# Kernel optimization log

Measured on AMD Instinct MI355X. Metric: run time of the kernel, lower is better.

The kernel has to match this reference:

```python
import jax, jax.numpy as jnp
import numpy as np

RES, K, H = 8192, 48, 128

def _layer_norm(x, g, b, eps=1e-5):
    mu = jnp.mean(x, axis=-1, keepdims=True)
    var = jnp.var(x, axis=-1, keepdims=True)
    return (x - mu) * jax.lax.rsqrt(var + eps) * g + b

def _gelu(x):
    return jax.nn.gelu(x, approximate=False)  # torch default exact GELU

def setup_inputs() -> dict:
    key = jax.random.key(0)
    ks = jax.random.split(key, 16)
    s = 0.05
    inp = {
        "node_h": jax.random.normal(ks[0], (RES, H), jnp.float32),
        "edge_h": jax.random.normal(ks[1], (RES, K, H), jnp.float32),
        "edge_idx": jax.random.randint(ks[2], (RES, K), 0, RES, jnp.int32),
        "seq_emb": jax.random.normal(ks[3], (RES, H), jnp.float32),
        "ar_mask": jax.random.uniform(ks[4], (RES, K), jnp.float32),
        # msg_mlp: Linear(4h,h) -> GELU -> Linear(h,h) -> GELU -> Linear(h,h)
        "mW1": jax.random.normal(ks[5], (4 * H, H), jnp.float32) * s,
        "mb1": jnp.zeros((H,), jnp.float32),
        "mW2": jax.random.normal(ks[6], (H, H), jnp.float32) * s,
        "mb2": jnp.zeros((H,), jnp.float32),
        "mW3": jax.random.normal(ks[7], (H, H), jnp.float32) * s,
        "mb3": jnp.zeros((H,), jnp.float32),
        # ff_node: Linear(h,4h) -> GELU -> Linear(4h,h)
        "fW1": jax.random.normal(ks[8], (H, 4 * H), jnp.float32) * s,
        "fb1": jnp.zeros((4 * H,), jnp.float32),
        "fW2": jax.random.normal(ks[9], (4 * H, H), jnp.float32) * s,
        "fb2": jnp.zeros((H,), jnp.float32),
        "g1": jnp.ones((H,), jnp.float32), "b1": jnp.zeros((H,), jnp.float32),
        "g2": jnp.ones((H,), jnp.float32), "b2": jnp.zeros((H,), jnp.float32),
    }
    return inp

def reference(node_h, edge_h, edge_idx, seq_emb, ar_mask,
              mW1, mb1, mW2, mb2, mW3, mb3,
              fW1, fb1, fW2, fb2, g1, b1, g2, b2):
    seq_j = seq_emb[edge_idx] * ar_mask[..., None]           # [res,k,h]
    e_dec = jnp.concatenate([edge_h, seq_j], axis=-1)        # [res,k,2h]
    h_j = node_h[edge_idx]                                   # [res,k,h]
    h_i = jnp.broadcast_to(node_h[:, None, :], (node_h.shape[0], edge_idx.shape[1], node_h.shape[1]))
    x = jnp.concatenate([h_i, h_j, e_dec], axis=-1)          # [res,k,4h]
    msg = _gelu(x @ mW1 + mb1)
    msg = _gelu(msg @ mW2 + mb2)
    msg = msg @ mW3 + mb3                                    # [res,k,h]
    agg = jnp.sum(msg, axis=1)                               # [res,h]
    h = _layer_norm(node_h + agg, g1, b1)
    ff = _gelu(h @ fW1 + fb1) @ fW2 + fb2
    h = _layer_norm(h + ff, g2, b2)
    return h
```

## Files before the change

### kernel.cpp

```cpp
#include <hip/hip_runtime.h>

#define KNB 48

typedef float  floatx4 __attribute__((ext_vector_type(4)));
typedef __bf16 bf16x8  __attribute__((ext_vector_type(8)));
typedef unsigned short ushort8  __attribute__((ext_vector_type(8)));
typedef unsigned short ushort4v __attribute__((ext_vector_type(4)));

__device__ __forceinline__ float bf2f(unsigned short b) {
  union { unsigned int u; float f; } v; v.u = ((unsigned int)b) << 16; return v.f;
}
__device__ __forceinline__ unsigned short f2bf(float f) {
  __bf16 h = (__bf16)f;
  union { __bf16 h; unsigned short u; } v; v.h = h; return v.u;
}
__device__ __forceinline__ float gelu_f(float x) {
  float u = x * (0.7978845608f + 0.0356774081f * x * x);
  float t = __builtin_amdgcn_exp2f(u * -2.8853900818f);
  return x * __builtin_amdgcn_rcpf(1.0f + t);
}

__global__ __launch_bounds__(256) void k0_transpose(
    const float* mW1, const float* mW2, const float* mW3,
    const float* fW1, const float* fW2,
    unsigned short* MT1, unsigned short* WT2, unsigned short* WT3,
    unsigned short* FWT1, unsigned short* FWT2) {
  __shared__ unsigned short tile[32][33];
  int b = blockIdx.x;
  const float* src; unsigned short* dst; int Kd, Nd, t;
  if (b < 64)       { src = mW1; dst = MT1;  Kd = 512; Nd = 128; t = b; }
  else if (b < 80)  { src = mW2; dst = WT2;  Kd = 128; Nd = 128; t = b - 64; }
  else if (b < 96)  { src = mW3; dst = WT3;  Kd = 128; Nd = 128; t = b - 80; }
  else if (b < 160) { src = fW1; dst = FWT1; Kd = 128; Nd = 512; t = b - 96; }
  else              { src = fW2; dst = FWT2; Kd = 512; Nd = 128; t = b - 160; }
  int tN = Nd >> 5;
  int tk = t / tN, tn = t % tN;
  int tx = threadIdx.x & 31, ty = threadIdx.x >> 5;
  for (int r = 0; r < 4; ++r) {
    int row = ty + r * 8;
    tile[row][tx] = f2bf(src[(size_t)(tk * 32 + row) * Nd + tn * 32 + tx]);
  }
  __syncthreads();
  for (int r = 0; r < 4; ++r) {
    int row = ty + r * 8;
    dst[(size_t)(tn * 32 + row) * Kd + tk * 32 + tx] = tile[tx][row];
  }
}

__global__ __launch_bounds__(256) void k1_nodepre(
    const float* node_h, const float* seq_emb,
    const unsigned short* MT1, const float* mb1,
    float* Apr, unsigned short* BS) {
  __shared__ __align__(16) unsigned short sX[2][32 * 128];
  int r0 = blockIdx.x * 32;
  int tid = threadIdx.x, lane = tid & 63, w = tid >> 6;
  int l15 = lane & 15, l16 = lane >> 4;

  for (int mset = 0; mset < 2; ++mset) {
    const float* src = mset ? (seq_emb + (size_t)r0 * 128) : (node_h + (size_t)r0 * 128);
    for (int k = 0; k < 4; ++k) {
      int f = tid + 256 * k;
      floatx4 v = ((const floatx4*)src)[f];
      int row = f >> 5, hc = f & 31, c = hc >> 1, half = hc & 1;
      ushort4v o;
      o[0] = f2bf(v[0]); o[1] = f2bf(v[1]); o[2] = f2bf(v[2]); o[3] = f2bf(v[3]);
      *(ushort4v*)((char*)&sX[mset][0] + row * 256 + ((c ^ (row & 7)) << 4) + half * 8) = o;
    }
  }
  __syncthreads();

  for (int q = 0; q < 6; ++q) {
    int job = w + 4 * q;
    int kind = job >> 3;
    int nt = job & 7;
    int colOff = (kind == 0) ? 0 : (kind == 1) ? 128 : 384;
    const unsigned short* X = sX[kind == 2 ? 1 : 0];
    bf16x8 wf[4];
    for (int kk = 0; kk < 4; ++kk)
      wf[kk] = *(const bf16x8*)(MT1 + (size_t)(nt * 16 + l15) * 512 + colOff + kk * 32 + l16 * 8);
    for (int mt = 0; mt < 2; ++mt) {
      floatx4 acc = {0.f, 0.f, 0.f, 0.f};
      for (int kk = 0; kk < 4; ++kk) {
        int row = mt * 16 + l15;
        int off = (kk * 64 + l16 * 16) ^ ((row & 7) << 4);
        bf16x8 a = *(const bf16x8*)((const char*)X + row * 256 + off);
        acc = __builtin_amdgcn_mfma_f32_16x16x32_bf16(a, wf[kk], acc, 0, 0, 0);
      }
      int col = nt * 16 + l15;
      for (int r = 0; r < 4; ++r) {
        int row = r0 + mt * 16 + l16 * 4 + r;
        if (kind == 0)      Apr[(size_t)row * 128 + col] = acc[r] + mb1[col];
        else if (kind == 1) BS[(size_t)row * 256 + col] = f2bf(acc[r]);
        else                BS[(size_t)row * 256 + 128 + col] = f2bf(acc[r]);
      }
    }
  }
}

__global__ __launch_bounds__(512) void k2_edge(
    const float* edge_h, const int* edge_idx, const float* ar_mask,
    const unsigned short* MT1, const unsigned short* WT2, const unsigned short* WT3,
    const float* mb2, const float* mb3,
    const float* Apr, const unsigned short* BS,
    float* agg) {
  __shared__ __align__(16) unsigned short sE[96 * 128];
  __shared__ __align__(16) unsigned short sT[96 * 128];
  int i0 = blockIdx.x * 2;
  int tid = threadIdx.x, lane = tid & 63, w = tid >> 6;
  int l15 = lane & 15, l16 = lane >> 4;
  int rb = (l16 & 1) * 4;
  int colw = w * 16 + l15;
  int cp = ((colw >> 3) << 4) | ((l15 & 7) << 1);

  const float* eb = edge_h + (size_t)i0 * KNB * 128;
#pragma unroll
  for (int k = 0; k < 6; ++k) {
    int f = tid + 512 * k;
    floatx4 v = ((const floatx4*)eb)[f];
    int row = f >> 5, hc = f & 31, c = hc >> 1, half = hc & 1;
    ushort4v o;
    o[0] = f2bf(v[0]); o[1] = f2bf(v[1]); o[2] = f2bf(v[2]); o[3] = f2bf(v[3]);
    *(ushort4v*)((char*)sE + row * 256 + ((c ^ (row & 7)) << 4) + half * 8) = o;
  }
#pragma unroll
  for (int k = 0; k < 3; ++k) {
    int u = tid + 512 * k;
    int e = u >> 4, c8 = u & 15;
    int j = edge_idx[(size_t)i0 * KNB + e];
    float m = ar_mask[(size_t)i0 * KNB + e];
    int i = i0 + (e >= 48 ? 1 : 0);
    const floatx4* ap = (const floatx4*)(Apr + (size_t)i * 128 + c8 * 8);
    floatx4 a0 = ap[0], a1 = ap[1];
    ushort8 vb = *(const ushort8*)(BS + (size_t)j * 256 + c8 * 8);
    ushort8 vs = *(const ushort8*)(BS + (size_t)j * 256 + 128 + c8 * 8);
    ushort8 res;
#pragma unroll
    for (int x = 0; x < 4; ++x)
      res[x] = f2bf(a0[x] + bf2f(vb[x]) + m * bf2f(vs[x]));
#pragma unroll
    for (int x = 0; x < 4; ++x)
      res[4 + x] = f2bf(a1[x] + bf2f(vb[4 + x]) + m * bf2f(vs[4 + x]));
    *(ushort8*)((char*)sT + e * 256 + ((c8 ^ (e & 7)) * 16)) = res;
  }
  __syncthreads();

  {
    bf16x8 wf[4];
#pragma unroll
    for (int kk = 0; kk < 4; ++kk)
      wf[kk] = *(const bf16x8*)(MT1 + (size_t)colw * 512 + 256 + kk * 32 + l16 * 8);
    for (int mt = 0; mt < 6; ++mt) {
      floatx4 acc = {0.f,0.f,0.f,0.f};
#pragma unroll
      for (int kk = 0; kk < 4; ++kk) {
        int row = mt * 16 + l15;
        int off = (kk * 64 + l16 * 16) ^ ((row & 7) << 4);
        bf16x8 a = *(const bf16x8*)((const char*)sE + row * 256 + off);
        acc = __builtin_amdgcn_mfma_f32_16x16x32_bf16(a, wf[kk], acc, 0, 0, 0);
      }
      char* base = (char*)sT + (mt * 16 + l16 * 4) * 256;
#pragma unroll
      for (int r = 0; r < 4; ++r) {
        char* p = base + r * 256 + (cp ^ ((rb + r) << 4));
        float g = bf2f(*(unsigned short*)p);
        *(unsigned short*)p = f2bf(gelu_f(acc[r] + g));
      }
    }
  }
  __syncthreads();

  {
    bf16x8 wf[4];
#pragma unroll
    for (int kk = 0; kk < 4; ++kk)
      wf[kk] = *(const bf16x8*)(WT2 + (size_t)colw * 128 + kk * 32 + l16 * 8);
    float bb = mb2[colw];
    for (int mt = 0; mt < 6; ++mt) {
      floatx4 acc = {0.f,0.f,0.f,0.f};
#pragma unroll
      for (int kk = 0; kk < 4; ++kk) {
        int row = mt * 16 + l15;
        int off = (kk * 64 + l16 * 16) ^ ((row & 7) << 4);
        bf16x8 a = *(const bf16x8*)((const char*)sT + row * 256 + off);
        acc = __builtin_amdgcn_mfma_f32_16x16x32_bf16(a, wf[kk], acc, 0, 0, 0);
      }
      char* base = (char*)sE + (mt * 16 + l16 * 4) * 256;
#pragma unroll
      for (int r = 0; r < 4; ++r) {
        char* p = base + r * 256 + (cp ^ ((rb + r) << 4));
        *(unsigned short*)p = f2bf(gelu_f(acc[r] + bb));
      }
    }
  }
  __syncthreads();

  {
    bf16x8 wf[4];
#pragma unroll
    for (int kk = 0; kk < 4; ++kk)
      wf[kk] = *(const bf16x8*)(WT3 + (size_t)colw * 128 + kk * 32 + l16 * 8);
#pragma unroll
    for (int half = 0; half < 2; ++half) {
      float agga[4] = {0.f,0.f,0.f,0.f};
      for (int mt3 = 0; mt3 < 3; ++mt3) {
        int mt = half * 3 + mt3;
        floatx4 acc = {0.f,0.f,0.f,0.f};
#pragma unroll
        for (int kk = 0; kk < 4; ++kk) {
          int row = mt * 16 + l15;
          int off = (kk * 64 + l16 * 16) ^ ((row & 7) << 4);
          bf16x8 a = *(const bf16x8*)((const char*)sE + row * 256 + off);
          acc = __builtin_amdgcn_mfma_f32_16x16x32_bf16(a, wf[kk], acc, 0, 0, 0);
        }
#pragma unroll
        for (int r = 0; r < 4; ++r) agga[r] += acc[r];
      }
      float s = agga[0] + agga[1] + agga[2] + agga[3];
      s += __shfl_xor(s, 16);
      s += __shfl_xor(s, 32);
      if (lane < 16) {
        int col = w * 16 + lane;
        agg[(size_t)(i0 + half) * 128 + col] = s + 48.0f * mb3[col];
      }
    }
  }
}

__global__ __launch_bounds__(256) void k3_ff(
    const float* node_h, const float* agg,
    const unsigned short* FWT1, const unsigned short* FWT2,
    const float* fb1, const float* fb2,
    const float* g1, const float* b1,
    const float* g2, const float* b2,
    float* out) {
  __shared__ __align__(16) unsigned short sH[32 * 128];
  __shared__ __align__(16) unsigned short sT3[32 * 512];
  __shared__ float sP[32 * 128];
  int r0 = blockIdx.x * 32;
  int tid = threadIdx.x, lane = tid & 63, w = tid >> 6;
  int l15 = lane & 15, l16 = lane >> 4;

  {
    int row = tid >> 3;
    int c0 = (tid & 7) * 16;
    const floatx4* nh4 = (const floatx4*)(node_h + (size_t)(r0 + row) * 128 + c0);
    const floatx4* ag4 = (const floatx4*)(agg + (size_t)(r0 + row) * 128 + c0);
    float x[16]; float sum = 0.f, sum2 = 0.f;
#pragma unroll
    for (int q4 = 0; q4 < 4; ++q4) {
      floatx4 a = nh4[q4], g = ag4[q4];
#pragma unroll
      for (int j = 0; j < 4; ++j) {
        float xv = a[j] + g[j];
        x[q4 * 4 + j] = xv; sum += xv; sum2 += xv * xv;
      }
    }
    sum  += __shfl_xor(sum, 1);  sum  += __shfl_xor(sum, 2);  sum  += __shfl_xor(sum, 4);
    sum2 += __shfl_xor(sum2, 1); sum2 += __shfl_xor(sum2, 2); sum2 += __shfl_xor(sum2, 4);
    float mu = sum * (1.f / 128.f);
    float var = sum2 * (1.f / 128.f) - mu * mu;
    float rstd = rsqrtf(var + 1e-5f);
#pragma unroll
    for (int q = 0; q < 16; ++q) {
      int col = c0 + q;
      float h = (x[q] - mu) * rstd * g1[col] + b1[col];
      sP[row * 128 + col] = h;
      char* p = (char*)sH + row * 256 + ((((col >> 3) ^ (row & 7)) << 4) | ((col & 7) << 1));
      *(unsigned short*)p = f2bf(h);
    }
  }
  __syncthreads();

  for (int nq = 0; nq < 8; ++nq) {
    int nt = w * 8 + nq;
    bf16x8 wf[4];
    for (int kk = 0; kk < 4; ++kk)
      wf[kk] = *(const bf16x8*)(FWT1 + (size_t)(nt * 16 + l15) * 128 + kk * 32 + l16 * 8);
    for (int mt = 0; mt < 2; ++mt) {
      floatx4 acc = {0.f,0.f,0.f,0.f};
      for (int kk = 0; kk < 4; ++kk) {
        int row = mt * 16 + l15;
        int off = (kk * 64 + l16 * 16) ^ ((row & 7) << 4);
        bf16x8 a = *(const bf16x8*)((const char*)sH + row * 256 + off);
        acc = __builtin_amdgcn_mfma_f32_16x16x32_bf16(a, wf[kk], acc, 0, 0, 0);
      }
      int col = nt * 16 + l15;
      float bb = fb1[col];
      for (int r = 0; r < 4; ++r) {
        int row = mt * 16 + l16 * 4 + r;
        char* p = (char*)sT3 + row * 1024 + ((((col >> 3) ^ (row & 7)) << 4) | ((col & 7) << 1));
        *(unsigned short*)p = f2bf(gelu_f(acc[r] + bb));
      }
    }
  }
  __syncthreads();

  for (int n = 0; n < 2; ++n) {
    int nt = 2 * w + n;
    for (int mt = 0; mt < 2; ++mt) {
      floatx4 acc = {0.f,0.f,0.f,0.f};
      for (int kk = 0; kk < 16; ++kk) {
        int row = mt * 16 + l15;
        int off = (kk * 64 + l16 * 16) ^ ((row & 7) << 4);
        bf16x8 a = *(const bf16x8*)((const char*)sT3 + row * 1024 + off);
        bf16x8 b = *(const bf16x8*)(FWT2 + (size_t)(nt * 16 + l15) * 512 + kk * 32 + l16 * 8);
        acc = __builtin_amdgcn_mfma_f32_16x16x32_bf16(a, b, acc, 0, 0, 0);
      }
      int col = nt * 16 + l15;
      float bb = fb2[col];
      for (int r = 0; r < 4; ++r) {
        int row = mt * 16 + l16 * 4 + r;
        sP[row * 128 + col] += acc[r] + bb;
      }
    }
  }
  __syncthreads();

  {
    int row = tid >> 3;
    int c0 = (tid & 7) * 16;
    float x[16]; float sum = 0.f, sum2 = 0.f;
#pragma unroll
    for (int q = 0; q < 16; ++q) {
      float xv = sP[row * 128 + c0 + q];
      x[q] = xv; sum += xv; sum2 += xv * xv;
    }
    sum  += __shfl_xor(sum, 1);  sum  += __shfl_xor(sum, 2);  sum  += __shfl_xor(sum, 4);
    sum2 += __shfl_xor(sum2, 1); sum2 += __shfl_xor(sum2, 2); sum2 += __shfl_xor(sum2, 4);
    float mu = sum * (1.f / 128.f);
    float var = sum2 * (1.f / 128.f) - mu * mu;
    float rstd = rsqrtf(var + 1e-5f);
#pragma unroll
    for (int q = 0; q < 16; ++q) {
      int col = c0 + q;
      out[(size_t)(r0 + row) * 128 + col] = (x[q] - mu) * rstd * g2[col] + b2[col];
    }
  }
}

extern "C" void kernel_launch(void* const* d_in, const int* in_sizes, int n_in,
                              void* d_out, int out_size, void* d_ws, size_t ws_size,
                              hipStream_t stream) {
  const float* node_h  = (const float*)d_in[0];
  const float* edge_h  = (const float*)d_in[1];
  const int*   edge_idx= (const int*)d_in[2];
  const float* seq_emb = (const float*)d_in[3];
  const float* ar_mask = (const float*)d_in[4];
  const float* mW1 = (const float*)d_in[5];
  const float* mb1 = (const float*)d_in[6];
  const float* mW2 = (const float*)d_in[7];
  const float* mb2 = (const float*)d_in[8];
  const float* mW3 = (const float*)d_in[9];
  const float* mb3 = (const float*)d_in[10];
  const float* fW1 = (const float*)d_in[11];
  const float* fb1 = (const float*)d_in[12];
  const float* fW2 = (const float*)d_in[13];
  const float* fb2 = (const float*)d_in[14];
  const float* g1  = (const float*)d_in[15];
  const float* b1  = (const float*)d_in[16];
  const float* g2  = (const float*)d_in[17];
  const float* b2  = (const float*)d_in[18];

  char* ws = (char*)d_ws;
  unsigned short* MT1  = (unsigned short*)(ws + 0);
  unsigned short* WT2  = (unsigned short*)(ws + 131072);
  unsigned short* WT3  = (unsigned short*)(ws + 163840);
  unsigned short* FWT1 = (unsigned short*)(ws + 196608);
  unsigned short* FWT2 = (unsigned short*)(ws + 327680);
  float*          Apr  = (float*)(ws + 458752);
  unsigned short* BS   = (unsigned short*)(ws + 4653056);
  float*          agg  = (float*)(ws + 8847360);

  hipLaunchKernelGGL(k0_transpose, dim3(224), dim3(256), 0, stream,
                     mW1, mW2, mW3, fW1, fW2, MT1, WT2, WT3, FWT1, FWT2);
  hipLaunchKernelGGL(k1_nodepre, dim3(256), dim3(256), 0, stream,
                     node_h, seq_emb, MT1, mb1, Apr, BS);
  hipLaunchKernelGGL(k2_edge, dim3(4096), dim3(512), 0, stream,
                     edge_h, edge_idx, ar_mask, MT1, WT2, WT3, mb2, mb3,
                     Apr, BS, agg);
  hipLaunchKernelGGL(k3_ff, dim3(256), dim3(256), 0, stream,
                     node_h, agg, FWT1, FWT2, fb1, fb2, g1, b1, g2, b2,
                     (float*)d_out);
}
```

Baseline: 139.5 us.

## Retile edge MLP waves to 48 rows x 32 cols with split accumulators

In the edge kernel, each wave previously covered all 96 edge rows for one 16-column tile. It now covers one residue's 48 rows for two 16-column tiles, so each A fragment loaded from LDS feeds two MFMAs and LDS read traffic roughly halves. Each column tile also uses two independent accumulators, which breaks the MFMA dependency chain and exposes more instruction-level parallelism. The price is higher register use from two weight fragment sets, partly addressed by a launch_bounds occupancy hint of (512, 6). The final per-residue reduction no longer needs a loop over halves.

Result: slower. 191.8 us (+37.5%).

```diff
diff --git a/kernel.cpp b/kernel.cpp
--- a/kernel.cpp
+++ b/kernel.cpp
@@ -19,6 +19,8 @@
   float t = __builtin_amdgcn_exp2f(u * -2.8853900818f);
   return x * __builtin_amdgcn_rcpf(1.0f + t);
 }
+
+#define MFMA16(a, b, c) __builtin_amdgcn_mfma_f32_16x16x32_bf16((a), (b), (c), 0, 0, 0)
 
 __global__ __launch_bounds__(256) void k0_transpose(
     const float* mW1, const float* mW2, const float* mW3,
@@ -84,7 +86,7 @@
         int row = mt * 16 + l15;
         int off = (kk * 64 + l16 * 16) ^ ((row & 7) << 4);
         bf16x8 a = *(const bf16x8*)((const char*)X + row * 256 + off);
-        acc = __builtin_amdgcn_mfma_f32_16x16x32_bf16(a, wf[kk], acc, 0, 0, 0);
+        acc = MFMA16(a, wf[kk], acc);
       }
       int col = nt * 16 + l15;
       for (int r = 0; r < 4; ++r) {
@@ -97,7 +99,7 @@
   }
 }
 
-__global__ __launch_bounds__(512) void k2_edge(
+__global__ __launch_bounds__(512, 6) void k2_edge(
     const float* edge_h, const int* edge_idx, const float* ar_mask,
     const unsigned short* MT1, const unsigned short* WT2, const unsigned short* WT3,
     const float* mb2, const float* mb3,
@@ -108,9 +110,13 @@
   int i0 = blockIdx.x * 2;
   int tid = threadIdx.x, lane = tid & 63, w = tid >> 6;
   int l15 = lane & 15, l16 = lane >> 4;
+  int h = w >> 2;
+  int ntp = w & 3;
+  int R0 = h * 48;
+  int cA = ntp * 32 + l15, cB = cA + 16;
   int rb = (l16 & 1) * 4;
-  int colw = w * 16 + l15;
-  int cp = ((colw >> 3) << 4) | ((l15 & 7) << 1);
+  int cpA = ((cA >> 3) << 4) | ((l15 & 7) << 1);
+  int cpB = ((cB >> 3) << 4) | ((l15 & 7) << 1);
 
   const float* eb = edge_h + (size_t)i0 * KNB * 128;
 #pragma unroll
@@ -145,83 +151,113 @@
   __syncthreads();
 
   {
-    bf16x8 wf[4];
-#pragma unroll
-    for (int kk = 0; kk < 4; ++kk)
-      wf[kk] = *(const bf16x8*)(MT1 + (size_t)colw * 512 + 256 + kk * 32 + l16 * 8);
-    for (int mt = 0; mt < 6; ++mt) {
-      floatx4 acc = {0.f,0.f,0.f,0.f};
+    bf16x8 wfA[4], wfB[4];
+#pragma unroll
+    for (int kk = 0; kk < 4; ++kk) {
+      wfA[kk] = *(const bf16x8*)(MT1 + (size_t)cA * 512 + 256 + kk * 32 + l16 * 8);
+      wfB[kk] = *(const bf16x8*)(MT1 + (size_t)cB * 512 + 256 + kk * 32 + l16 * 8);
+    }
+#pragma unroll
+    for (int mt = 0; mt < 3; ++mt) {
+      bf16x8 af[4];
 #pragma unroll
       for (int kk = 0; kk < 4; ++kk) {
-        int row = mt * 16 + l15;
-        int off = (kk * 64 + l16 * 16) ^ ((row & 7) << 4);
-        bf16x8 a = *(const bf16x8*)((const char*)sE + row * 256 + off);
-        acc = __builtin_amdgcn_mfma_f32_16x16x32_bf16(a, wf[kk], acc, 0, 0, 0);
-      }
-      char* base = (char*)sT + (mt * 16 + l16 * 4) * 256;
-#pragma unroll
-      for (int r = 0; r < 4; ++r) {
-        char* p = base + r * 256 + (cp ^ ((rb + r) << 4));
-        float g = bf2f(*(unsigned short*)p);
-        *(unsigned short*)p = f2bf(gelu_f(acc[r] + g));
+        int row = R0 + mt * 16 + l15;
+        int off = (kk * 64 + l16 * 16) ^ ((row & 7) << 4);
+        af[kk] = *(const bf16x8*)((const char*)sE + row * 256 + off);
+      }
+      floatx4 aA0 = {0.f,0.f,0.f,0.f}, aA1 = {0.f,0.f,0.f,0.f};
+      floatx4 aB0 = {0.f,0.f,0.f,0.f}, aB1 = {0.f,0.f,0.f,0.f};
+      aA0 = MFMA16(af[0], wfA[0], aA0); aB0 = MFMA16(af[0], wfB[0], aB0);
+      aA1 = MFMA16(af[1], wfA[1], aA1); aB1 = MFMA16(af[1], wfB[1], aB1);
+      aA0 = MFMA16(af[2], wfA[2], aA0); aB0 = MFMA16(af[2], wfB[2], aB0);
+      aA1 = MFMA16(af[3], wfA[3], aA1); aB1 = MFMA16(af[3], wfB[3], aB1);
+      char* base = (char*)sT + (R0 + mt * 16 + l16 * 4) * 256;
+#pragma unroll
+      for (int r = 0; r < 4; ++r) {
+        int sw = (rb + r) << 4;
+        char* pA = base + r * 256 + (cpA ^ sw);
+        char* pB = base + r * 256 + (cpB ^ sw);
+        float gA = bf2f(*(unsigned short*)pA);
+        float gB = bf2f(*(unsigned short*)pB);
+        *(unsigned short*)pA = f2bf(gelu_f(aA0[r] + aA1[r] + gA));
+        *(unsigned short*)pB = f2bf(gelu_f(aB0[r] + aB1[r] + gB));
       }
     }
   }
   __syncthreads();
 
   {
-    bf16x8 wf[4];
-#pragma unroll
-    for (int kk = 0; kk < 4; ++kk)
-      wf[kk] = *(const bf16x8*)(WT2 + (size_t)colw * 128 + kk * 32 + l16 * 8);
-    float bb = mb2[colw];
-    for (int mt = 0; mt < 6; ++mt) {
-      floatx4 acc = {0.f,0.f,0.f,0.f};
+    bf16x8 wfA[4], wfB[4];
+#pragma unroll
+    for (int kk = 0; kk < 4; ++kk) {
+      wfA[kk] = *(const bf16x8*)(WT2 + (size_t)cA * 128 + kk * 32 + l16 * 8);
+      wfB[kk] = *(const bf16x8*)(WT2 + (size_t)cB * 128 + kk * 32 + l16 * 8);
+    }
+    float bbA = mb2[cA], bbB = mb2[cB];
+#pragma unroll
+    for (int mt = 0; mt < 3; ++mt) {
+      bf16x8 af[4];
 #pragma unroll
       for (int kk = 0; kk < 4; ++kk) {
-        int row = mt * 16 + l15;
-        int off = (kk * 64 + l16 * 16) ^ ((row & 7) << 4);
-        bf16x8 a = *(const bf16x8*)((const char*)sT + row * 256 + off);
-        acc = __builtin_amdgcn_mfma_f32_16x16x32_bf16(a, wf[kk], acc, 0, 0, 0);
-      }
-      char* base = (char*)sE + (mt * 16 + l16 * 4) * 256;
-#pragma unroll
-      for (int r = 0; r < 4; ++r) {
-        char* p = base + r * 256 + (cp ^ ((rb + r) << 4));
-        *(unsigned short*)p = f2bf(gelu_f(acc[r] + bb));
+        int row = R0 + mt * 16 + l15;
+        int off = (kk * 64 + l16 * 16) ^ ((row & 7) << 4);
+        af[kk] = *(const bf16x8*)((const char*)sT + row * 256 + off);
+      }
+      floatx4 aA0 = {0.f,0.f,0.f,0.f}, aA1 = {0.f,0.f,0.f,0.f};
+      floatx4 aB0 = {0.f,0.f,0.f,0.f}, aB1 = {0.f,0.f,0.f,0.f};
+      aA0 = MFMA16(af[0], wfA[0], aA0); aB0 = MFMA16(af[0], wfB[0], aB0);
+      aA1 = MFMA16(af[1], wfA[1], aA1); aB1 = MFMA16(af[1], wfB[1], aB1);
+      aA0 = MFMA16(af[2], wfA[2], aA0); aB0 = MFMA16(af[2], wfB[2], aB0);
+      aA1 = MFMA16(af[3], wfA[3], aA1); aB1 = MFMA16(af[3], wfB[3], aB1);
+      char* base = (char*)sE + (R0 + mt * 16 + l16 * 4) * 256;
+#pragma unroll
+      for (int r = 0; r < 4; ++r) {
+        int sw = (rb + r) << 4;
+        *(unsigned short*)(base + r * 256 + (cpA ^ sw)) = f2bf(gelu_f(aA0[r] + aA1[r] + bbA));
+        *(unsigned short*)(base + r * 256 + (cpB ^ sw)) = f2bf(gelu_f(aB0[r] + aB1[r] + bbB));
       }
     }
   }
   __syncthreads();
 
   {
-    bf16x8 wf[4];
-#pragma unroll
-    for (int kk = 0; kk < 4; ++kk)
-      wf[kk] = *(const bf16x8*)(WT3 + (size_t)colw * 128 + kk * 32 + l16 * 8);
-#pragma unroll
-    for (int half = 0; half < 2; ++half) {
-      float agga[4] = {0.f,0.f,0.f,0.f};
-      for (int mt3 = 0; mt3 < 3; ++mt3) {
-        int mt = half * 3 + mt3;
-        floatx4 acc = {0.f,0.f,0.f,0.f};
-#pragma unroll
-        for (int kk = 0; kk < 4; ++kk) {
-          int row = mt * 16 + l15;
-          int off = (kk * 64 + l16 * 16) ^ ((row & 7) << 4);
-          bf16x8 a = *(const bf16x8*)((const char*)sE + row * 256 + off);
-          acc = __builtin_amdgcn_mfma_f32_16x16x32_bf16(a, wf[kk], acc, 0, 0, 0);
-        }
-#pragma unroll
-        for (int r = 0; r < 4; ++r) agga[r] += acc[r];
-      }
-      float s = agga[0] + agga[1] + agga[2] + agga[3];
-      s += __shfl_xor(s, 16);
-      s += __shfl_xor(s, 32);
-      if (lane < 16) {
-        int col = w * 16 + lane;
-        agg[(size_t)(i0 + half) * 128 + col] = s + 48.0f * mb3[col];
-      }
+    bf16x8 wfA[4], wfB[4];
+#pragma unroll
+    for (int kk = 0; kk < 4; ++kk) {
+      wfA[kk] = *(const bf16x8*)(WT3 + (size_t)cA * 128 + kk * 32 + l16 * 8);
+      wfB[kk] = *(const bf16x8*)(WT3 + (size_t)cB * 128 + kk * 32 + l16 * 8);
+    }
+    float sumA[4] = {0.f,0.f,0.f,0.f}, sumB[4] = {0.f,0.f,0.f,0.f};
+#pragma unroll
+    for (int mt = 0; mt < 3; ++mt) {
+      bf16x8 af[4];
+#pragma unroll
+      for (int kk = 0; kk < 4; ++kk) {
+        int row = R0 + mt * 16 + l15;
+        int off = (kk * 64 + l16 * 16) ^ ((row & 7) << 4);
+        af[kk] = *(const bf16x8*)((const char*)sE + row * 256 + off);
+      }
+      floatx4 aA0 = {0.f,0.f,0.f,0.f}, aA1 = {0.f,0.f,0.f,0.f};
+      floatx4 aB0 = {0.f,0.f,0.f,0.f}, aB1 = {0.f,0.f,0.f,0.f};
+      aA0 = MFMA16(af[0], wfA[0], aA0); aB0 = MFMA16(af[0], wfB[0], aB0);
+      aA1 = MFMA16(af[1], wfA[1], aA1); aB1 = MFMA16(af[1], wfB[1], aB1);
+      aA0 = MFMA16(af[2], wfA[2], aA0); aB0 = MFMA16(af[2], wfB[2], aB0);
+      aA1 = MFMA16(af[3], wfA[3], aA1); aB1 = MFMA16(af[3], wfB[3], aB1);
+#pragma unroll
+      for (int r = 0; r < 4; ++r) {
+        sumA[r] += aA0[r] + aA1[r];
+        sumB[r] += aB0[r] + aB1[r];
+      }
+    }
+    float sA = sumA[0] + sumA[1] + sumA[2] + sumA[3];
+    float sB = sumB[0] + sumB[1] + sumB[2] + sumB[3];
+    sA += __shfl_xor(sA, 16); sA += __shfl_xor(sA, 32);
+    sB += __shfl_xor(sB, 16); sB += __shfl_xor(sB, 32);
+    if (lane < 16) {
+      int colA = ntp * 32 + lane, colB = colA + 16;
+      agg[(size_t)(i0 + h) * 128 + colA] = sA + 48.0f * mb3[colA];
+      agg[(size_t)(i0 + h) * 128 + colB] = sB + 48.0f * mb3[colB];
     }
   }
 }
@@ -282,7 +318,7 @@
         int row = mt * 16 + l15;
         int off = (kk * 64 + l16 * 16) ^ ((row & 7) << 4);
         bf16x8 a = *(const bf16x8*)((const char*)sH + row * 256 + off);
-        acc = __builtin_amdgcn_mfma_f32_16x16x32_bf16(a, wf[kk], acc, 0, 0, 0);
+        acc = MFMA16(a, wf[kk], acc);
       }
       int col = nt * 16 + l15;
       float bb = fb1[col];
@@ -304,7 +340,7 @@
         int off = (kk * 64 + l16 * 16) ^ ((row & 7) << 4);
         bf16x8 a = *(const bf16x8*)((const char*)sT3 + row * 1024 + off);
         bf16x8 b = *(const bf16x8*)(FWT2 + (size_t)(nt * 16 + l15) * 512 + kk * 32 + l16 * 8);
-        acc = __builtin_amdgcn_mfma_f32_16x16x32_bf16(a, b, acc, 0, 0, 0);
+        acc = MFMA16(a, b, acc);
       }
       int col = nt * 16 + l15;
       float bb = fb2[col];
```

## Make edge kernel persistent over four node pairs with register prefetch of next tile

Applied to the files above, without the earlier changes.

The edge kernel now processes four consecutive node pairs per block instead of one, which cuts the grid by a factor of four. For the next pair it prefetches edge_h, edge_idx and ar_mask into registers while the current pair's three MFMA layers run. The goal is to overlap the large edge_h stream with compute and amortise block launch and weight-fragment setup. The cost is more registers for the prefetch buffers, an extra barrier per iteration, and fewer blocks to spread across CUs; launch_bounds(512,4) is set to limit register use.

Result: slower. 147.2 us (+5.5%).

```diff
diff --git a/kernel.cpp b/kernel.cpp
--- a/kernel.cpp
+++ b/kernel.cpp
@@ -1,6 +1,7 @@
 #include <hip/hip_runtime.h>
 
 #define KNB 48
+#define NT  4
 
 typedef float  floatx4 __attribute__((ext_vector_type(4)));
 typedef __bf16 bf16x8  __attribute__((ext_vector_type(8)));
@@ -19,6 +20,8 @@
   float t = __builtin_amdgcn_exp2f(u * -2.8853900818f);
   return x * __builtin_amdgcn_rcpf(1.0f + t);
 }
+
+#define MFMA16(a, b, c) __builtin_amdgcn_mfma_f32_16x16x32_bf16((a), (b), (c), 0, 0, 0)
 
 __global__ __launch_bounds__(256) void k0_transpose(
     const float* mW1, const float* mW2, const float* mW3,
@@ -84,7 +87,7 @@
         int row = mt * 16 + l15;
         int off = (kk * 64 + l16 * 16) ^ ((row & 7) << 4);
         bf16x8 a = *(const bf16x8*)((const char*)X + row * 256 + off);
-        acc = __builtin_amdgcn_mfma_f32_16x16x32_bf16(a, wf[kk], acc, 0, 0, 0);
+        acc = MFMA16(a, wf[kk], acc);
       }
       int col = nt * 16 + l15;
       for (int r = 0; r < 4; ++r) {
@@ -97,7 +100,7 @@
   }
 }
 
-__global__ __launch_bounds__(512) void k2_edge(
+__global__ __launch_bounds__(512, 4) void k2_edge(
     const float* edge_h, const int* edge_idx, const float* ar_mask,
     const unsigned short* MT1, const unsigned short* WT2, const unsigned short* WT3,
     const float* mb2, const float* mb3,
@@ -105,124 +108,156 @@
     float* agg) {
   __shared__ __align__(16) unsigned short sE[96 * 128];
   __shared__ __align__(16) unsigned short sT[96 * 128];
-  int i0 = blockIdx.x * 2;
   int tid = threadIdx.x, lane = tid & 63, w = tid >> 6;
   int l15 = lane & 15, l16 = lane >> 4;
   int rb = (l16 & 1) * 4;
   int colw = w * 16 + l15;
   int cp = ((colw >> 3) << 4) | ((l15 & 7) << 1);
 
-  const float* eb = edge_h + (size_t)i0 * KNB * 128;
-#pragma unroll
-  for (int k = 0; k < 6; ++k) {
-    int f = tid + 512 * k;
-    floatx4 v = ((const floatx4*)eb)[f];
-    int row = f >> 5, hc = f & 31, c = hc >> 1, half = hc & 1;
-    ushort4v o;
-    o[0] = f2bf(v[0]); o[1] = f2bf(v[1]); o[2] = f2bf(v[2]); o[3] = f2bf(v[3]);
-    *(ushort4v*)((char*)sE + row * 256 + ((c ^ (row & 7)) << 4) + half * 8) = o;
-  }
-#pragma unroll
-  for (int k = 0; k < 3; ++k) {
-    int u = tid + 512 * k;
-    int e = u >> 4, c8 = u & 15;
-    int j = edge_idx[(size_t)i0 * KNB + e];
-    float m = ar_mask[(size_t)i0 * KNB + e];
-    int i = i0 + (e >= 48 ? 1 : 0);
-    const floatx4* ap = (const floatx4*)(Apr + (size_t)i * 128 + c8 * 8);
-    floatx4 a0 = ap[0], a1 = ap[1];
-    ushort8 vb = *(const ushort8*)(BS + (size_t)j * 256 + c8 * 8);
-    ushort8 vs = *(const ushort8*)(BS + (size_t)j * 256 + 128 + c8 * 8);
-    ushort8 res;
-#pragma unroll
-    for (int x = 0; x < 4; ++x)
-      res[x] = f2bf(a0[x] + bf2f(vb[x]) + m * bf2f(vs[x]));
-#pragma unroll
-    for (int x = 0; x < 4; ++x)
-      res[4 + x] = f2bf(a1[x] + bf2f(vb[4 + x]) + m * bf2f(vs[4 + x]));
-    *(ushort8*)((char*)sT + e * 256 + ((c8 ^ (e & 7)) * 16)) = res;
-  }
-  __syncthreads();
+  int p0 = blockIdx.x * NT;
+
+  floatx4 ev[6];
+  int   jr[3];
+  float mr[3];
 
   {
-    bf16x8 wf[4];
-#pragma unroll
-    for (int kk = 0; kk < 4; ++kk)
-      wf[kk] = *(const bf16x8*)(MT1 + (size_t)colw * 512 + 256 + kk * 32 + l16 * 8);
-    for (int mt = 0; mt < 6; ++mt) {
-      floatx4 acc = {0.f,0.f,0.f,0.f};
-#pragma unroll
-      for (int kk = 0; kk < 4; ++kk) {
-        int row = mt * 16 + l15;
-        int off = (kk * 64 + l16 * 16) ^ ((row & 7) << 4);
-        bf16x8 a = *(const bf16x8*)((const char*)sE + row * 256 + off);
-        acc = __builtin_amdgcn_mfma_f32_16x16x32_bf16(a, wf[kk], acc, 0, 0, 0);
-      }
-      char* base = (char*)sT + (mt * 16 + l16 * 4) * 256;
-#pragma unroll
-      for (int r = 0; r < 4; ++r) {
-        char* p = base + r * 256 + (cp ^ ((rb + r) << 4));
-        float g = bf2f(*(unsigned short*)p);
-        *(unsigned short*)p = f2bf(gelu_f(acc[r] + g));
-      }
-    }
-  }
-  __syncthreads();
-
-  {
-    bf16x8 wf[4];
-#pragma unroll
-    for (int kk = 0; kk < 4; ++kk)
-      wf[kk] = *(const bf16x8*)(WT2 + (size_t)colw * 128 + kk * 32 + l16 * 8);
-    float bb = mb2[colw];
-    for (int mt = 0; mt < 6; ++mt) {
-      floatx4 acc = {0.f,0.f,0.f,0.f};
-#pragma unroll
-      for (int kk = 0; kk < 4; ++kk) {
-        int row = mt * 16 + l15;
-        int off = (kk * 64 + l16 * 16) ^ ((row & 7) << 4);
-        bf16x8 a = *(const bf16x8*)((const char*)sT + row * 256 + off);
-        acc = __builtin_amdgcn_mfma_f32_16x16x32_bf16(a, wf[kk], acc, 0, 0, 0);
-      }
-      char* base = (char*)sE + (mt * 16 + l16 * 4) * 256;
-#pragma unroll
-      for (int r = 0; r < 4; ++r) {
-        char* p = base + r * 256 + (cp ^ ((rb + r) << 4));
-        *(unsigned short*)p = f2bf(gelu_f(acc[r] + bb));
-      }
-    }
-  }
-  __syncthreads();
-
-  {
-    bf16x8 wf[4];
-#pragma unroll
-    for (int kk = 0; kk < 4; ++kk)
-      wf[kk] = *(const bf16x8*)(WT3 + (size_t)colw * 128 + kk * 32 + l16 * 8);
-#pragma unroll
-    for (int half = 0; half < 2; ++half) {
-      float agga[4] = {0.f,0.f,0.f,0.f};
-      for (int mt3 = 0; mt3 < 3; ++mt3) {
-        int mt = half * 3 + mt3;
+    const float* eb = edge_h + (size_t)(p0 * 2) * KNB * 128;
+#pragma unroll
+    for (int k = 0; k < 6; ++k) ev[k] = ((const floatx4*)eb)[tid + 512 * k];
+#pragma unroll
+    for (int k = 0; k < 3; ++k) {
+      int e = (tid + 512 * k) >> 4;
+      jr[k] = edge_idx[(size_t)(p0 * 2) * KNB + e];
+      mr[k] = ar_mask[(size_t)(p0 * 2) * KNB + e];
+    }
+  }
+
+  for (int t = 0; t < NT; ++t) {
+    int i0 = (p0 + t) * 2;
+
+#pragma unroll
+    for (int k = 0; k < 6; ++k) {
+      int f = tid + 512 * k;
+      floatx4 v = ev[k];
+      int row = f >> 5, hc = f & 31, c = hc >> 1, half = hc & 1;
+      ushort4v o;
+      o[0] = f2bf(v[0]); o[1] = f2bf(v[1]); o[2] = f2bf(v[2]); o[3] = f2bf(v[3]);
+      *(ushort4v*)((char*)sE + row * 256 + ((c ^ (row & 7)) << 4) + half * 8) = o;
+    }
+#pragma unroll
+    for (int k = 0; k < 3; ++k) {
+      int u = tid + 512 * k;
+      int e = u >> 4, c8 = u & 15;
+      int j = jr[k]; float m = mr[k];
+      int i = i0 + (e >= 48 ? 1 : 0);
+      const floatx4* ap = (const floatx4*)(Apr + (size_t)i * 128 + c8 * 8);
+      floatx4 a0 = ap[0], a1 = ap[1];
+      ushort8 vb = *(const ushort8*)(BS + (size_t)j * 256 + c8 * 8);
+      ushort8 vs = *(const ushort8*)(BS + (size_t)j * 256 + 128 + c8 * 8);
+      ushort8 res;
+#pragma unroll
+      for (int x = 0; x < 4; ++x)
+        res[x] = f2bf(a0[x] + bf2f(vb[x]) + m * bf2f(vs[x]));
+#pragma unroll
+      for (int x = 0; x < 4; ++x)
+        res[4 + x] = f2bf(a1[x] + bf2f(vb[4 + x]) + m * bf2f(vs[4 + x]));
+      *(ushort8*)((char*)sT + e * 256 + ((c8 ^ (e & 7)) * 16)) = res;
+    }
+    __syncthreads();
+
+    if (t + 1 < NT) {
+      const float* eb = edge_h + (size_t)((p0 + t + 1) * 2) * KNB * 128;
+#pragma unroll
+      for (int k = 0; k < 6; ++k) ev[k] = ((const floatx4*)eb)[tid + 512 * k];
+#pragma unroll
+      for (int k = 0; k < 3; ++k) {
+        int e = (tid + 512 * k) >> 4;
+        jr[k] = edge_idx[(size_t)((p0 + t + 1) * 2) * KNB + e];
+        mr[k] = ar_mask[(size_t)((p0 + t + 1) * 2) * KNB + e];
+      }
+    }
+
+    {
+      bf16x8 wf[4];
+#pragma unroll
+      for (int kk = 0; kk < 4; ++kk)
+        wf[kk] = *(const bf16x8*)(MT1 + (size_t)colw * 512 + 256 + kk * 32 + l16 * 8);
+      for (int mt = 0; mt < 6; ++mt) {
         floatx4 acc = {0.f,0.f,0.f,0.f};
 #pragma unroll
         for (int kk = 0; kk < 4; ++kk) {
           int row = mt * 16 + l15;
           int off = (kk * 64 + l16 * 16) ^ ((row & 7) << 4);
           bf16x8 a = *(const bf16x8*)((const char*)sE + row * 256 + off);
-          acc = __builtin_amdgcn_mfma_f32_16x16x32_bf16(a, wf[kk], acc, 0, 0, 0);
-        }
-#pragma unroll
-        for (int r = 0; r < 4; ++r) agga[r] += acc[r];
-      }
-      float s = agga[0] + agga[1] + agga[2] + agga[3];
-      s += __shfl_xor(s, 16);
-      s += __shfl_xor(s, 32);
-      if (lane < 16) {
-        int col = w * 16 + lane;
-        agg[(size_t)(i0 + half) * 128 + col] = s + 48.0f * mb3[col];
-      }
-    }
+          acc = MFMA16(a, wf[kk], acc);
+        }
+        char* base = (char*)sT + (mt * 16 + l16 * 4) * 256;
+#pragma unroll
+        for (int r = 0; r < 4; ++r) {
+          char* p = base + r * 256 + (cp ^ ((rb + r) << 4));
+          float g = bf2f(*(unsigned short*)p);
+          *(unsigned short*)p = f2bf(gelu_f(acc[r] + g));
+        }
+      }
+    }
+    __syncthreads();
+
+    {
+      bf16x8 wf[4];
+#pragma unroll
+      for (int kk = 0; kk < 4; ++kk)
+        wf[kk] = *(const bf16x8*)(WT2 + (size_t)colw * 128 + kk * 32 + l16 * 8);
+      float bb = mb2[colw];
+      for (int mt = 0; mt < 6; ++mt) {
+        floatx4 acc = {0.f,0.f,0.f,0.f};
+#pragma unroll
+        for (int kk = 0; kk < 4; ++kk) {
+          int row = mt * 16 + l15;
+          int off = (kk * 64 + l16 * 16) ^ ((row & 7) << 4);
+          bf16x8 a = *(const bf16x8*)((const char*)sT + row * 256 + off);
+          acc = MFMA16(a, wf[kk], acc);
+        }
+        char* base = (char*)sE + (mt * 16 + l16 * 4) * 256;
+#pragma unroll
+        for (int r = 0; r < 4; ++r) {
+          char* p = base + r * 256 + (cp ^ ((rb + r) << 4));
+          *(unsigned short*)p = f2bf(gelu_f(acc[r] + bb));
+        }
+      }
+    }
+    __syncthreads();
+
+    {
+      bf16x8 wf[4];
+#pragma unroll
+      for (int kk = 0; kk < 4; ++kk)
+        wf[kk] = *(const bf16x8*)(WT3 + (size_t)colw * 128 + kk * 32 + l16 * 8);
+#pragma unroll
+      for (int half = 0; half < 2; ++half) {
+        float agga[4] = {0.f,0.f,0.f,0.f};
+        for (int mt3 = 0; mt3 < 3; ++mt3) {
+          int mt = half * 3 + mt3;
+          floatx4 acc = {0.f,0.f,0.f,0.f};
+#pragma unroll
+          for (int kk = 0; kk < 4; ++kk) {
+            int row = mt * 16 + l15;
+            int off = (kk * 64 + l16 * 16) ^ ((row & 7) << 4);
+            bf16x8 a = *(const bf16x8*)((const char*)sE + row * 256 + off);
+            acc = MFMA16(a, wf[kk], acc);
+          }
+#pragma unroll
+          for (int r = 0; r < 4; ++r) agga[r] += acc[r];
+        }
+        float s = agga[0] + agga[1] + agga[2] + agga[3];
+        s += __shfl_xor(s, 16);
+        s += __shfl_xor(s, 32);
+        if (lane < 16) {
+          int col = w * 16 + lane;
+          agg[(size_t)(i0 + half) * 128 + col] = s + 48.0f * mb3[col];
+        }
+      }
+    }
+    __syncthreads();
   }
 }
 
@@ -282,7 +317,7 @@
         int row = mt * 16 + l15;
         int off = (kk * 64 + l16 * 16) ^ ((row & 7) << 4);
         bf16x8 a = *(const bf16x8*)((const char*)sH + row * 256 + off);
-        acc = __builtin_amdgcn_mfma_f32_16x16x32_bf16(a, wf[kk], acc, 0, 0, 0);
+        acc = MFMA16(a, wf[kk], acc);
       }
       int col = nt * 16 + l15;
       float bb = fb1[col];
@@ -304,7 +339,7 @@
         int off = (kk * 64 + l16 * 16) ^ ((row & 7) << 4);
         bf16x8 a = *(const bf16x8*)((const char*)sT3 + row * 1024 + off);
         bf16x8 b = *(const bf16x8*)(FWT2 + (size_t)(nt * 16 + l15) * 512 + kk * 32 + l16 * 8);
-        acc = __builtin_amdgcn_mfma_f32_16x16x32_bf16(a, b, acc, 0, 0, 0);
+        acc = MFMA16(a, b, acc);
       }
       int col = nt * 16 + l15;
       float bb = fb2[col];
@@ -375,7 +410,7 @@
                      mW1, mW2, mW3, fW1, fW2, MT1, WT2, WT3, FWT1, FWT2);
   hipLaunchKernelGGL(k1_nodepre, dim3(256), dim3(256), 0, stream,
                      node_h, seq_emb, MT1, mb1, Apr, BS);
-  hipLaunchKernelGGL(k2_edge, dim3(4096), dim3(512), 0, stream,
+  hipLaunchKernelGGL(k2_edge, dim3(4096 / NT), dim3(512), 0, stream,
                      edge_h, edge_idx, ar_mask, MT1, WT2, WT3, mb2, mb3,
                      Apr, BS, agg);
   hipLaunchKernelGGL(k3_ff, dim3(256), dim3(256), 0, stream,
```
